# Kernel optimization log

Measured on AMD Instinct MI355X. Metric: run time of the kernel, lower is better.

Reference implementation:

```python
import jax, jax.numpy as jnp
import numpy as np

BLOCK = 512  # circulant block size

def block_circulant_matmul(x, w):
    """Block-circulant linear layer (CirCNN-style), no bias.
    x: (..., p*BLOCK); w: (q, p, BLOCK) -> out: (..., q*BLOCK).
    Each (q,p) block is a circulant matrix applied via FFT (circular conv).
    """
    q, p, b = w.shape
    xb = x.reshape(x.shape[:-1] + (p, b))            # (..., p, b)
    Xf = jnp.fft.rfft(xb, axis=-1)                    # (..., p, b//2+1) complex
    Wf = jnp.fft.rfft(w, axis=-1)                     # (q, p, b//2+1)
    Yf = jnp.einsum('...pf,qpf->...qf', Xf, Wf)       # sum over input blocks
    y = jnp.fft.irfft(Yf, n=b, axis=-1)               # (..., q, b)
    return y.reshape(x.shape[:-1] + (q * b,))

def setup_inputs() -> dict:
    key = jax.random.key(0)
    k1, k2, k3, k4 = jax.random.split(key, 4)
    d_model, d_ff, b = 2048, 5632, BLOCK
    p_in, q_ff = d_model // b, d_ff // b              # 4, 11
    scale = 1.0 / np.sqrt(d_model)
    x = jax.random.normal(k1, (4, 4096, d_model), dtype=jnp.float32)
    w_gate = jax.random.normal(k2, (q_ff, p_in, b), dtype=jnp.float32) * scale
    w_up   = jax.random.normal(k3, (q_ff, p_in, b), dtype=jnp.float32) * scale
    w_down = jax.random.normal(k4, (p_in, q_ff, b), dtype=jnp.float32) * (1.0 / np.sqrt(d_ff))
    return {"x": x, "w_gate": w_gate, "w_up": w_up, "w_down": w_down}

def reference(x, w_gate, w_up, w_down):
    # SwiGLU: down( SiLU(gate(x)) * up(x) ); dropout=0 -> identity
    gate = jax.nn.silu(block_circulant_matmul(x, w_gate))
    up = block_circulant_matmul(x, w_up)
    return block_circulant_matmul(gate * up, w_down)
```

## Files before the change

### kernel.cpp

```cpp
#include <hip/hip_runtime.h>
#include <hip/hip_fp16.h>
#include <math.h>


__device__ __forceinline__ int swz(int n) { return n ^ ((n >> 3) & 15); }

struct Tw { float t0r[7], t0i[7], t1r[7], t1i[7]; };

__device__ __forceinline__ void make_tw(int l, Tw& T)
{
    float c0, s0;
    __sincosf(-6.283185307179586f * (float)l * (1.0f/512.0f), &s0, &c0);
    float pr = c0, pi = s0;
    T.t0r[0] = pr; T.t0i[0] = pi;
#pragma unroll
    for (int m = 1; m < 7; ++m) {
        float nr = pr*c0 - pi*s0, ni = pr*s0 + pi*c0;
        pr = nr; pi = ni;
        T.t0r[m] = pr; T.t0i[m] = pi;
    }
    float c1, s1;
    __sincosf(-6.283185307179586f * (float)(l >> 3) * (1.0f/64.0f), &s1, &c1);
    pr = c1; pi = s1;
    T.t1r[0] = pr; T.t1i[0] = pi;
#pragma unroll
    for (int m = 1; m < 7; ++m) {
        float nr = pr*c1 - pi*s1, ni = pr*s1 + pi*c1;
        pr = nr; pi = ni;
        T.t1r[m] = pr; T.t1i[m] = pi;
    }
}

template<bool INV>
__device__ __forceinline__ void dft8(float xr[8], float xi[8])
{
    const float C = 0.70710678118654752f;
    float tr[4], ti[4], ur[4], ui[4];
#pragma unroll
    for (int q = 0; q < 4; ++q) {
        tr[q] = xr[q] + xr[q+4];  ti[q] = xi[q] + xi[q+4];
        ur[q] = xr[q] - xr[q+4];  ui[q] = xi[q] - xi[q+4];
    }
    {
        float xx = ur[1], yy = ui[1];
        if (!INV) { ur[1] = C*(xx+yy); ui[1] = C*(yy-xx); }
        else      { ur[1] = C*(xx-yy); ui[1] = C*(xx+yy); }
    }
    {
        float xx = ur[2], yy = ui[2];
        if (!INV) { ur[2] = yy;  ui[2] = -xx; }
        else      { ur[2] = -yy; ui[2] = xx; }
    }
    {
        float xx = ur[3], yy = ui[3];
        if (!INV) { ur[3] = C*(yy-xx);  ui[3] = -C*(xx+yy); }
        else      { ur[3] = -C*(xx+yy); ui[3] = C*(xx-yy); }
    }
    {
        float s0r=tr[0]+tr[2], s0i=ti[0]+ti[2];
        float d0r=tr[0]-tr[2], d0i=ti[0]-ti[2];
        float s1r=tr[1]+tr[3], s1i=ti[1]+ti[3];
        float e1r=tr[1]-tr[3], e1i=ti[1]-ti[3];
        float d1r, d1i;
        if (!INV) { d1r = e1i;  d1i = -e1r; } else { d1r = -e1i; d1i = e1r; }
        xr[0]=s0r+s1r; xi[0]=s0i+s1i;
        xr[2]=d0r+d1r; xi[2]=d0i+d1i;
        xr[4]=s0r-s1r; xi[4]=s0i-s1i;
        xr[6]=d0r-d1r; xi[6]=d0i-d1i;
    }
    {
        float s0r=ur[0]+ur[2], s0i=ui[0]+ui[2];
        float d0r=ur[0]-ur[2], d0i=ui[0]-ui[2];
        float s1r=ur[1]+ur[3], s1i=ui[1]+ui[3];
        float e1r=ur[1]-ur[3], e1i=ui[1]-ui[3];
        float d1r, d1i;
        if (!INV) { d1r = e1i;  d1i = -e1r; } else { d1r = -e1i; d1i = e1r; }
        xr[1]=s0r+s1r; xi[1]=s0i+s1i;
        xr[3]=d0r+d1r; xi[3]=d0i+d1i;
        xr[5]=s0r-s1r; xi[5]=s0i-s1i;
        xr[7]=d0r-d1r; xi[7]=d0i-d1i;
    }
}

template<bool INV>
__device__ __forceinline__ void twiddle7(float xr[8], float xi[8],
                                         const float* tr, const float* ti)
{
#pragma unroll
    for (int m = 1; m < 8; ++m) {
        float wr = tr[m-1], wi = INV ? -ti[m-1] : ti[m-1];
        float nr = xr[m]*wr - xi[m]*wi, ni = xr[m]*wi + xi[m]*wr;
        xr[m]=nr; xi[m]=ni;
    }
}

template<bool INV>
__device__ __forceinline__ void fft512_r8(float2* wk, int l, const Tw& T)
{
    float xr[8], xi[8];
#pragma unroll
    for (int q = 0; q < 8; ++q) { float2 v = wk[swz(l + 64*q)]; xr[q]=v.x; xi[q]=v.y; }
    dft8<INV>(xr, xi);
    twiddle7<INV>(xr, xi, T.t0r, T.t0i);
#pragma unroll
    for (int m = 0; m < 8; ++m) wk[swz(8*l + m)] = make_float2(xr[m], xi[m]);
#pragma unroll
    for (int q = 0; q < 8; ++q) { float2 v = wk[swz(l + 64*q)]; xr[q]=v.x; xi[q]=v.y; }
    dft8<INV>(xr, xi);
    twiddle7<INV>(xr, xi, T.t1r, T.t1i);
    {
        const int base = 64*(l>>3) + (l&7);
#pragma unroll
        for (int m = 0; m < 8; ++m) wk[swz(base + 8*m)] = make_float2(xr[m], xi[m]);
    }
#pragma unroll
    for (int q = 0; q < 8; ++q) { float2 v = wk[swz(l + 64*q)]; xr[q]=v.x; xi[q]=v.y; }
    dft8<INV>(xr, xi);
#pragma unroll
    for (int m = 0; m < 8; ++m) wk[swz(l + 64*m)] = make_float2(xr[m], xi[m]);
}

template<bool INV>
__device__ __forceinline__ void fft512_r8_head(float2* wk, int l, const Tw& T,
                                               float xr[8], float xi[8])
{
#pragma unroll
    for (int q = 0; q < 8; ++q) { float2 v = wk[swz(l + 64*q)]; xr[q]=v.x; xi[q]=v.y; }
    dft8<INV>(xr, xi);
    twiddle7<INV>(xr, xi, T.t0r, T.t0i);
#pragma unroll
    for (int m = 0; m < 8; ++m) wk[swz(8*l + m)] = make_float2(xr[m], xi[m]);
#pragma unroll
    for (int q = 0; q < 8; ++q) { float2 v = wk[swz(l + 64*q)]; xr[q]=v.x; xi[q]=v.y; }
    dft8<INV>(xr, xi);
    twiddle7<INV>(xr, xi, T.t1r, T.t1i);
    {
        const int base = 64*(l>>3) + (l&7);
#pragma unroll
        for (int m = 0; m < 8; ++m) wk[swz(base + 8*m)] = make_float2(xr[m], xi[m]);
    }
#pragma unroll
    for (int q = 0; q < 8; ++q) { float2 v = wk[swz(l + 64*q)]; xr[q]=v.x; xi[q]=v.y; }
    dft8<INV>(xr, xi);
}

template<bool INV>
__device__ __forceinline__ void fft512_r8_tail(float2* wk, int l, const Tw& T,
                                               float xr[8], float xi[8])
{
    dft8<INV>(xr, xi);
    twiddle7<INV>(xr, xi, T.t0r, T.t0i);
#pragma unroll
    for (int m = 0; m < 8; ++m) wk[swz(8*l + m)] = make_float2(xr[m], xi[m]);
#pragma unroll
    for (int q = 0; q < 8; ++q) { float2 v = wk[swz(l + 64*q)]; xr[q]=v.x; xi[q]=v.y; }
    dft8<INV>(xr, xi);
    twiddle7<INV>(xr, xi, T.t1r, T.t1i);
    {
        const int base = 64*(l>>3) + (l&7);
#pragma unroll
        for (int m = 0; m < 8; ++m) wk[swz(base + 8*m)] = make_float2(xr[m], xi[m]);
    }
#pragma unroll
    for (int q = 0; q < 8; ++q) { float2 v = wk[swz(l + 64*q)]; xr[q]=v.x; xi[q]=v.y; }
    dft8<INV>(xr, xi);
#pragma unroll
    for (int m = 0; m < 8; ++m) wk[swz(l + 64*m)] = make_float2(xr[m], xi[m]);
}

__global__ __launch_bounds__(64) void wf_prep(const float* __restrict__ wg,
                                              const float* __restrict__ wu,
                                              const float* __restrict__ wd,
                                              float2* __restrict__ wsp)
{
    __shared__ float2 wk[512];
    const int t = threadIdx.x;
    Tw T; make_tw(t, T);
    const int b = blockIdx.x;
    const float* src = (b < 44) ? (wg + (size_t)b * 512)
                     : (b < 88) ? (wu + (size_t)(b - 44) * 512)
                                : (wd + (size_t)(b - 88) * 512);
    float2* dst = wsp + (size_t)b * 257;

#pragma unroll
    for (int i = 0; i < 8; ++i) { int n = t + 64*i; wk[swz(n)] = make_float2(src[n], 0.f); }
    fft512_r8<false>(wk, t, T);
    const float sc = 1.0f / 512.0f;
#pragma unroll
    for (int i = 0; i < 5; ++i) {
        int k = t + 64*i;
        if (k <= 256) { float2 z = wk[swz(k)]; dst[k] = make_float2(sc*z.x, sc*z.y); }
    }
}

__global__ __launch_bounds__(256) void bcffn(const float* __restrict__ x,
                                             const float2* __restrict__ wsp,
                                             float* __restrict__ out)
{
    __shared__ float2  sWork[4 * 512];
    __shared__ __half2 sXf[4][257];
    __shared__ __half2 sHf[11][257];

    const int tid = threadIdx.x;
    const int t = tid & 63, w = tid >> 6;
    const size_t row = blockIdx.x;

    Tw T; make_tw(t, T);

    const float2* Wg = wsp;
    const float2* Wu = wsp + 44 * 257;
    const float2* Wd = wsp + 88 * 257;

    float2* wk = sWork + (w << 9);

    if (w < 2) {
        const float4* xa = (const float4*)(x + row * 2048 + (size_t)(2*w)   * 512);
        const float4* xb = (const float4*)(x + row * 2048 + (size_t)(2*w+1) * 512);
#pragma unroll
        for (int u = 0; u < 2; ++u) {
            int e = t + 64*u;
            float4 a = xa[e], b = xb[e];
            int n = 4*e;
            wk[swz(n+0)] = make_float2(a.x, b.x);
            wk[swz(n+1)] = make_float2(a.y, b.y);
            wk[swz(n+2)] = make_float2(a.z, b.z);
            wk[swz(n+3)] = make_float2(a.w, b.w);
        }
        fft512_r8<false>(wk, t, T);
#pragma unroll
        for (int u = 0; u < 5; ++u) {
            int k = t + 64*u;
            if (k <= 256) {
                float2 z = wk[swz(k)], m = wk[swz((512 - k) & 511)];
                sXf[2*w][k]   = __floats2half2_rn(0.5f*(z.x + m.x), 0.5f*(z.y - m.y));
                sXf[2*w+1][k] = __floats2half2_rn(0.5f*(z.y + m.y), 0.5f*(m.x - z.x));
            }
        }
    }
    __syncthreads();

    auto einsum_gu = [&](int q) {
#pragma unroll
        for (int u = 0; u < 5; ++u) {
            int k = t + 64*u;
            if (k <= 256) {
                float gr=0.f, gi=0.f, ur_=0.f, ui_=0.f;
#pragma unroll
                for (int p = 0; p < 4; ++p) {
                    float2 X = __half22float2(sXf[p][k]);
                    float2 a = Wg[(q*4 + p)*257 + k];
                    float2 b = Wu[(q*4 + p)*257 + k];
                    gr  += X.x*a.x - X.y*a.y;  gi  += X.x*a.y + X.y*a.x;
                    ur_ += X.x*b.x - X.y*b.y;  ui_ += X.x*b.y + X.y*b.x;
                }
                wk[swz(k)] = make_float2(gr - ui_, gi + ur_);
                if (k != 0 && k != 256)
                    wk[swz(512 - k)] = make_float2(gr + ui_, ur_ - gi);
            }
        }
    };

    {
        const int qa = w, qb = w + 4;
        float har[8];
        float xr[8], xi[8];

        einsum_gu(qa);
        fft512_r8_head<true>(wk, t, T, xr, xi);
#pragma unroll
        for (int u = 0; u < 8; ++u)
            har[u] = xr[u] * xi[u] / (1.f + __expf(-xr[u]));

        einsum_gu(qb);
        fft512_r8_head<true>(wk, t, T, xr, xi);
#pragma unroll
        for (int u = 0; u < 8; ++u) {
            float hb = xr[u] * xi[u] / (1.f + __expf(-xr[u]));
            xr[u] = har[u];  xi[u] = hb;
        }
        fft512_r8_tail<false>(wk, t, T, xr, xi);
#pragma unroll
        for (int u = 0; u < 5; ++u) {
            int k = t + 64*u;
            if (k <= 256) {
                float2 z = wk[swz(k)], m = wk[swz((512 - k) & 511)];
                sHf[qa][k] = __floats2half2_rn(0.5f*(z.x + m.x), 0.5f*(z.y - m.y));
                sHf[qb][k] = __floats2half2_rn(0.5f*(z.y + m.y), 0.5f*(m.x - z.x));
            }
        }

        if (w < 3) {
            const int qc = w + 8;
            einsum_gu(qc);
            fft512_r8_head<true>(wk, t, T, xr, xi);
#pragma unroll
            for (int u = 0; u < 8; ++u) {
                xr[u] = xr[u] * xi[u] / (1.f + __expf(-xr[u]));
                xi[u] = 0.f;
            }
            fft512_r8_tail<false>(wk, t, T, xr, xi);
#pragma unroll
            for (int u = 0; u < 5; ++u) {
                int k = t + 64*u;
                if (k <= 256) {
                    float2 v = wk[swz(k)];
                    sHf[qc][k] = __floats2half2_rn(v.x, v.y);
                }
            }
        }
    }
    __syncthreads();

    float Zr[5] = {0.f,0.f,0.f,0.f,0.f};
    float Zi[5] = {0.f,0.f,0.f,0.f,0.f};
#pragma unroll
    for (int u = 0; u < 5; ++u) {
        int k = t + 64*u;
        if (k <= 256) {
            float zr = 0.f, zi = 0.f;
#pragma unroll
            for (int q = 0; q < 11; ++q) {
                float2 H = __half22float2(sHf[q][k]);
                float2 d = Wd[(w*11 + q)*257 + k];
                zr += H.x*d.x - H.y*d.y;
                zi += H.x*d.y + H.y*d.x;
            }
            Zr[u] = zr; Zi[u] = zi;
        }
    }
    if (w >= 2) {
#pragma unroll
        for (int u = 0; u < 5; ++u) {
            int k = t + 64*u;
            if (k <= 256) sXf[w-2][k] = __floats2half2_rn(Zr[u], Zi[u]);
        }
    }
    __syncthreads();
    if (w < 2) {
#pragma unroll
        for (int u = 0; u < 5; ++u) {
            int k = t + 64*u;
            if (k <= 256) {
                float2 zb = __half22float2(sXf[w][k]);
                wk[swz(k)] = make_float2(Zr[u] - zb.y, Zi[u] + zb.x);
                if (k != 0 && k != 256)
                    wk[swz(512 - k)] = make_float2(Zr[u] + zb.y, zb.x - Zi[u]);
            }
        }
        fft512_r8<true>(wk, t, T);
        float4* oa = (float4*)(out + row * 2048 + (size_t)w       * 512);
        float4* ob = (float4*)(out + row * 2048 + (size_t)(w + 2) * 512);
#pragma unroll
        for (int u = 0; u < 2; ++u) {
            int e = t + 64*u, n = 4*e;
            float2 v0 = wk[swz(n)],   v1 = wk[swz(n+1)];
            float2 v2 = wk[swz(n+2)], v3 = wk[swz(n+3)];
            oa[e] = make_float4(v0.x, v1.x, v2.x, v3.x);
            ob[e] = make_float4(v0.y, v1.y, v2.y, v3.y);
        }
    }
}

extern "C" void kernel_launch(void* const* d_in, const int* in_sizes, int n_in,
                              void* d_out, int out_size, void* d_ws, size_t ws_size,
                              hipStream_t stream)
{
    (void)n_in; (void)out_size; (void)ws_size;
    const float* x  = (const float*)d_in[0];
    const float* wg = (const float*)d_in[1];
    const float* wu = (const float*)d_in[2];
    const float* wd = (const float*)d_in[3];
    float2* wsp = (float2*)d_ws;
    float*  out = (float*)d_out;

    const int rows = in_sizes[0] / 2048;

    wf_prep<<<132, 64, 0, stream>>>(wg, wu, wd, wsp);
    bcffn<<<rows, 256, 0, stream>>>(x, wsp, out);
}
```

Baseline: 561.4 us.

## Interleave two inverse FFT heads per wave with separate shared buffers

Gives each wave two shared-memory work buffers and runs the first two inverse FFT heads (gate/up blocks qa and qb) in one interleaved pass, so the two independent transforms can overlap their LDS traffic and arithmetic. The leftover q blocks move from waves 0-2 to waves 1-3, and the final inverse FFT moves from waves 0-1 to waves 2-3, to even out per-wave work. The SiLU division is replaced by a reciprocal multiply. Shared memory per block doubles and register pressure rises, which may lower occupancy.

```diff
diff --git a/kernel.cpp b/kernel.cpp
--- a/kernel.cpp
+++ b/kernel.cpp
@@ -145,6 +145,47 @@
 }
 
 template<bool INV>
+__device__ __forceinline__ void fft512_r8_head2(float2* wkA, float2* wkB, int l,
+                                                const Tw& T,
+                                                float xrA[8], float xiA[8],
+                                                float xrB[8], float xiB[8])
+{
+#pragma unroll
+    for (int q = 0; q < 8; ++q) { float2 v = wkA[swz(l + 64*q)]; xrA[q]=v.x; xiA[q]=v.y; }
+#pragma unroll
+    for (int q = 0; q < 8; ++q) { float2 v = wkB[swz(l + 64*q)]; xrB[q]=v.x; xiB[q]=v.y; }
+    dft8<INV>(xrA, xiA);
+    twiddle7<INV>(xrA, xiA, T.t0r, T.t0i);
+    dft8<INV>(xrB, xiB);
+    twiddle7<INV>(xrB, xiB, T.t0r, T.t0i);
+#pragma unroll
+    for (int m = 0; m < 8; ++m) wkA[swz(8*l + m)] = make_float2(xrA[m], xiA[m]);
+#pragma unroll
+    for (int m = 0; m < 8; ++m) wkB[swz(8*l + m)] = make_float2(xrB[m], xiB[m]);
+#pragma unroll
+    for (int q = 0; q < 8; ++q) { float2 v = wkA[swz(l + 64*q)]; xrA[q]=v.x; xiA[q]=v.y; }
+#pragma unroll
+    for (int q = 0; q < 8; ++q) { float2 v = wkB[swz(l + 64*q)]; xrB[q]=v.x; xiB[q]=v.y; }
+    dft8<INV>(xrA, xiA);
+    twiddle7<INV>(xrA, xiA, T.t1r, T.t1i);
+    dft8<INV>(xrB, xiB);
+    twiddle7<INV>(xrB, xiB, T.t1r, T.t1i);
+    {
+        const int base = 64*(l>>3) + (l&7);
+#pragma unroll
+        for (int m = 0; m < 8; ++m) wkA[swz(base + 8*m)] = make_float2(xrA[m], xiA[m]);
+#pragma unroll
+        for (int m = 0; m < 8; ++m) wkB[swz(base + 8*m)] = make_float2(xrB[m], xiB[m]);
+    }
+#pragma unroll
+    for (int q = 0; q < 8; ++q) { float2 v = wkA[swz(l + 64*q)]; xrA[q]=v.x; xiA[q]=v.y; }
+#pragma unroll
+    for (int q = 0; q < 8; ++q) { float2 v = wkB[swz(l + 64*q)]; xrB[q]=v.x; xiB[q]=v.y; }
+    dft8<INV>(xrA, xiA);
+    dft8<INV>(xrB, xiB);
+}
+
+template<bool INV>
 __device__ __forceinline__ void fft512_r8_tail(float2* wk, int l, const Tw& T,
                                                float xr[8], float xi[8])
 {
@@ -197,7 +238,7 @@
                                              const float2* __restrict__ wsp,
                                              float* __restrict__ out)
 {
-    __shared__ float2  sWork[4 * 512];
+    __shared__ float2  sWork[8 * 512];
     __shared__ __half2 sXf[4][257];
     __shared__ __half2 sHf[11][257];
 
@@ -211,7 +252,8 @@
     const float2* Wu = wsp + 44 * 257;
     const float2* Wd = wsp + 88 * 257;
 
-    float2* wk = sWork + (w << 9);
+    float2* wkA = sWork + (w << 10);
+    float2* wkB = wkA + 512;
 
     if (w < 2) {
         const float4* xa = (const float4*)(x + row * 2048 + (size_t)(2*w)   * 512);
@@ -221,17 +263,17 @@
             int e = t + 64*u;
             float4 a = xa[e], b = xb[e];
             int n = 4*e;
-            wk[swz(n+0)] = make_float2(a.x, b.x);
-            wk[swz(n+1)] = make_float2(a.y, b.y);
-            wk[swz(n+2)] = make_float2(a.z, b.z);
-            wk[swz(n+3)] = make_float2(a.w, b.w);
-        }
-        fft512_r8<false>(wk, t, T);
+            wkA[swz(n+0)] = make_float2(a.x, b.x);
+            wkA[swz(n+1)] = make_float2(a.y, b.y);
+            wkA[swz(n+2)] = make_float2(a.z, b.z);
+            wkA[swz(n+3)] = make_float2(a.w, b.w);
+        }
+        fft512_r8<false>(wkA, t, T);
 #pragma unroll
         for (int u = 0; u < 5; ++u) {
             int k = t + 64*u;
             if (k <= 256) {
-                float2 z = wk[swz(k)], m = wk[swz((512 - k) & 511)];
+                float2 z = wkA[swz(k)], m = wkA[swz((512 - k) & 511)];
                 sXf[2*w][k]   = __floats2half2_rn(0.5f*(z.x + m.x), 0.5f*(z.y - m.y));
                 sXf[2*w+1][k] = __floats2half2_rn(0.5f*(z.y + m.y), 0.5f*(m.x - z.x));
             }
@@ -239,7 +281,7 @@
     }
     __syncthreads();
 
-    auto einsum_gu = [&](int q) {
+    auto einsum_gu = [&](int q, float2* wk) {
 #pragma unroll
         for (int u = 0; u < 5; ++u) {
             int k = t + 64*u;
@@ -262,48 +304,43 @@
 
     {
         const int qa = w, qb = w + 4;
-        float har[8];
-        float xr[8], xi[8];
-
-        einsum_gu(qa);
-        fft512_r8_head<true>(wk, t, T, xr, xi);
-#pragma unroll
-        for (int u = 0; u < 8; ++u)
-            har[u] = xr[u] * xi[u] / (1.f + __expf(-xr[u]));
-
-        einsum_gu(qb);
-        fft512_r8_head<true>(wk, t, T, xr, xi);
+        float xrA[8], xiA[8], xrB[8], xiB[8];
+
+        einsum_gu(qa, wkA);
+        einsum_gu(qb, wkB);
+        fft512_r8_head2<true>(wkA, wkB, t, T, xrA, xiA, xrB, xiB);
 #pragma unroll
         for (int u = 0; u < 8; ++u) {
-            float hb = xr[u] * xi[u] / (1.f + __expf(-xr[u]));
-            xr[u] = har[u];  xi[u] = hb;
-        }
-        fft512_r8_tail<false>(wk, t, T, xr, xi);
+            float hA = xrA[u] * xiA[u] * __frcp_rn(1.f + __expf(-xrA[u]));
+            float hB = xrB[u] * xiB[u] * __frcp_rn(1.f + __expf(-xrB[u]));
+            xrA[u] = hA;  xiA[u] = hB;
+        }
+        fft512_r8_tail<false>(wkA, t, T, xrA, xiA);
 #pragma unroll
         for (int u = 0; u < 5; ++u) {
             int k = t + 64*u;
             if (k <= 256) {
-                float2 z = wk[swz(k)], m = wk[swz((512 - k) & 511)];
+                float2 z = wkA[swz(k)], m = wkA[swz((512 - k) & 511)];
                 sHf[qa][k] = __floats2half2_rn(0.5f*(z.x + m.x), 0.5f*(z.y - m.y));
                 sHf[qb][k] = __floats2half2_rn(0.5f*(z.y + m.y), 0.5f*(m.x - z.x));
             }
         }
 
-        if (w < 3) {
-            const int qc = w + 8;
-            einsum_gu(qc);
-            fft512_r8_head<true>(wk, t, T, xr, xi);
+        if (w >= 1) {
+            const int qc = w + 7;
+            einsum_gu(qc, wkB);
+            fft512_r8_head<true>(wkB, t, T, xrB, xiB);
 #pragma unroll
             for (int u = 0; u < 8; ++u) {
-                xr[u] = xr[u] * xi[u] / (1.f + __expf(-xr[u]));
-                xi[u] = 0.f;
-            }
-            fft512_r8_tail<false>(wk, t, T, xr, xi);
+                xrB[u] = xrB[u] * xiB[u] * __frcp_rn(1.f + __expf(-xrB[u]));
+                xiB[u] = 0.f;
+            }
+            fft512_r8_tail<false>(wkB, t, T, xrB, xiB);
 #pragma unroll
             for (int u = 0; u < 5; ++u) {
                 int k = t + 64*u;
                 if (k <= 256) {
-                    float2 v = wk[swz(k)];
+                    float2 v = wkB[swz(k)];
                     sHf[qc][k] = __floats2half2_rn(v.x, v.y);
                 }
             }
@@ -328,33 +365,33 @@
             Zr[u] = zr; Zi[u] = zi;
         }
     }
-    if (w >= 2) {
+    if (w < 2) {
 #pragma unroll
         for (int u = 0; u < 5; ++u) {
             int k = t + 64*u;
-            if (k <= 256) sXf[w-2][k] = __floats2half2_rn(Zr[u], Zi[u]);
+            if (k <= 256) sXf[w][k] = __floats2half2_rn(Zr[u], Zi[u]);
         }
     }
     __syncthreads();
-    if (w < 2) {
+    if (w >= 2) {
 #pragma unroll
         for (int u = 0; u < 5; ++u) {
             int k = t + 64*u;
             if (k <= 256) {
-                float2 zb = __half22float2(sXf[w][k]);
-                wk[swz(k)] = make_float2(Zr[u] - zb.y, Zi[u] + zb.x);
+                float2 za = __half22float2(sXf[w-2][k]);
+                wkA[swz(k)] = make_float2(za.x - Zi[u], za.y + Zr[u]);
                 if (k != 0 && k != 256)
-                    wk[swz(512 - k)] = make_float2(Zr[u] + zb.y, zb.x - Zi[u]);
-            }
-        }
-        fft512_r8<true>(wk, t, T);
-        float4* oa = (float4*)(out + row * 2048 + (size_t)w       * 512);
-        float4* ob = (float4*)(out + row * 2048 + (size_t)(w + 2) * 512);
+                    wkA[swz(512 - k)] = make_float2(za.x + Zi[u], Zr[u] - za.y);
+            }
+        }
+        fft512_r8<true>(wkA, t, T);
+        float4* oa = (float4*)(out + row * 2048 + (size_t)(w - 2) * 512);
+        float4* ob = (float4*)(out + row * 2048 + (size_t)w       * 512);
 #pragma unroll
         for (int u = 0; u < 2; ++u) {
             int e = t + 64*u, n = 4*e;
-            float2 v0 = wk[swz(n)],   v1 = wk[swz(n+1)];
-            float2 v2 = wk[swz(n+2)], v3 = wk[swz(n+3)];
+            float2 v0 = wkA[swz(n)],   v1 = wkA[swz(n+1)];
+            float2 v2 = wkA[swz(n+2)], v3 = wkA[swz(n+3)];
             oa[e] = make_float4(v0.x, v1.x, v2.x, v3.x);
             ob[e] = make_float4(v0.y, v1.y, v2.y, v3.y);
         }
```

After: 563.8 us. Within noise of the previous version (+0.4%).
